# Performance work log

Hardware: AMD Instinct MI355X
Metric: run time of the kernel (lower is better)

## Reference

```python
import jax, jax.numpy as jnp
import numpy as np


def setup_inputs() -> dict:
    key = jax.random.key(0)
    k1, k2, k3 = jax.random.split(key, 3)
    B, K, OUT, IN = 8192, 8, 1024, 1024
    bound = (6.0 / (IN * OUT)) ** 0.5
    x = jax.random.normal(k1, (B, IN), dtype=jnp.float32)
    expert_weights = jax.random.uniform(k2, (B, K), dtype=jnp.float32)
    weight = jax.random.uniform(k3, (K, OUT, IN), dtype=jnp.float32, minval=-bound, maxval=bound)
    bias = jnp.zeros((K, OUT), dtype=jnp.float32)
    return {"x": x, "expert_weights": expert_weights, "weight": weight, "bias": bias}


def reference(x, expert_weights, weight, bias):
    # Mathematically identical to: blended_W = einsum('bk,koi->boi'); bmm(blended_W, x)
    # but avoids materializing the [B,out,in] intermediate: apply each expert's
    # linear map then blend with routing weights (contraction reassociation).
    per_expert = jnp.einsum('bi,koi->bko', x, weight)        # [B, K, out]
    y = jnp.einsum('bk,bko->bo', expert_weights, per_expert)  # [B, out]
    y = y + expert_weights @ bias                             # blended bias [B, out]
    return y
```

## Files before the change

### kernel.cpp

```cpp
#include <hip/hip_runtime.h>
#include <hip/hip_bf16.h>

typedef __attribute__((ext_vector_type(8))) short short8;
typedef __attribute__((ext_vector_type(4))) float f32x4;

#define NDIM 1024
#define INDIM 1024
#define KEXP 8
#define BROWS 8192
#define NX (BROWS * INDIM)
#define NW (KEXP * NDIM * INDIM)

__device__ __forceinline__ unsigned int pack2bf(float a, float b) {
    __hip_bfloat162 h = __float22bfloat162_rn(make_float2(a, b));
    union { __hip_bfloat162 h; unsigned int u; } cv;
    cv.h = h;
    return cv.u;
}

__device__ __forceinline__ void gload16(const void* src, void* ldsdst) {
    __builtin_amdgcn_global_load_lds(
        (__attribute__((address_space(1))) void*)(src),
        (__attribute__((address_space(3))) void*)(ldsdst), 16, 0, 0);
}

__global__ void convert_bf16(const float* __restrict__ x, const float* __restrict__ w,
                             unsigned short* __restrict__ dst) {
    const long total = (long)NX + NW;
    const long stride = (long)gridDim.x * blockDim.x * 8;
    for (long i = ((long)blockIdx.x * blockDim.x + threadIdx.x) * 8; i < total; i += stride) {
        const float* s = (i < NX) ? (x + i) : (w + (i - NX));
        float4 a = ((const float4*)s)[0];
        float4 b = ((const float4*)s)[1];
        uint4 q;
        q.x = pack2bf(a.x, a.y); q.y = pack2bf(a.z, a.w);
        q.z = pack2bf(b.x, b.y); q.w = pack2bf(b.z, b.w);
        *(uint4*)(dst + i) = q;
    }
}

__global__ __launch_bounds__(512, 2)
void moe_gemm_fold(const unsigned short* __restrict__ xb,
                   const float* __restrict__ ew,
                   const unsigned short* __restrict__ Wp,
                   const float* __restrict__ bias,
                   float* __restrict__ out) {
    __shared__ __align__(16) unsigned short lds[2 * 32768];

    const int tid = threadIdx.x;
    const int bid = blockIdx.x;
    const int xcd = bid & 7;
    const int grp = bid >> 3;
    const int bt = xcd * 4 + (grp & 3);
    const int ot = grp >> 2;
    const int bbase = bt * 256;
    const int o_blk = ot * 32;

    const int w  = tid >> 6;
    const int l  = tid & 63;
    const int lr = l & 15;
    const int lg = l >> 4;
    const int wrow = (w >> 2) * 128;
    const int wcol = (w & 3) * 64;

    const int lrow = l >> 2;
    const int sg = (l & 3) ^ ((l >> 3) & 3);
    const int swz = (lr >> 1) & 3;

    int aoff[8][2], boff[4][2];
#pragma unroll
    for (int mf = 0; mf < 8; ++mf)
#pragma unroll
        for (int ks = 0; ks < 2; ++ks)
            aoff[mf][ks] = ks * 8192 + (wrow + mf * 16 + lr) * 32 + ((lg ^ swz) * 8);
#pragma unroll
    for (int nf = 0; nf < 4; ++nf)
#pragma unroll
        for (int ks = 0; ks < 2; ++ks)
            boff[nf][ks] = 16384 + ks * 8192 + (wcol + nf * 16 + lr) * 32 + ((lg ^ swz) * 8);

    auto stage4 = [&](int slot, int kt, int half) {
#pragma unroll
        for (int i = 0; i < 4; ++i) {
            const int id = w * 8 + half * 4 + i;
            unsigned short* dst = &lds[slot * 32768 + id * 512];
            const int sub = id & 15;
            const int col = kt * 64 + ((id >> 4) & 1) * 32 + sg * 8;
            if (id < 32) {
                gload16(Wp + (size_t)(lrow & 7) * (NDIM * INDIM)
                           + (size_t)(o_blk + sub * 2 + (lrow >> 3)) * INDIM + col, dst);
            } else {
                gload16(xb + (size_t)(bbase + sub * 16 + lrow) * INDIM + col, dst);
            }
        }
    };

    f32x4 acc[8][4];
#pragma unroll
    for (int mf = 0; mf < 8; ++mf)
#pragma unroll
        for (int nf = 0; nf < 4; ++nf) acc[mf][nf] = f32x4{0.f, 0.f, 0.f, 0.f};

    stage4(0, 0, 0);
    stage4(0, 0, 1);

#pragma unroll 1
    for (int kt = 0; kt < 16; ++kt) {
        const int cs = kt & 1;
        const bool doS = (kt + 1) < 16;

        asm volatile("s_waitcnt vmcnt(0)\n\ts_barrier" ::: "memory");

        const unsigned short* lb = &lds[cs * 32768];
        short8 alo[4], ahi[4], b0[4], b1[4];

#pragma unroll
        for (int m = 0; m < 4; ++m) alo[m] = *(const short8*)(lb + aoff[m][0]);
#pragma unroll
        for (int n = 0; n < 4; ++n) b0[n] = *(const short8*)(lb + boff[n][0]);
        if (doS) stage4(cs ^ 1, kt + 1, 0);
#pragma unroll
        for (int m = 0; m < 4; ++m) ahi[m] = *(const short8*)(lb + aoff[4 + m][0]);

        __builtin_amdgcn_s_setprio(1);
#pragma unroll
        for (int m = 0; m < 4; ++m)
#pragma unroll
            for (int n = 0; n < 4; ++n)
                acc[m][n] = __builtin_amdgcn_mfma_f32_16x16x32_bf16(alo[m], b0[n], acc[m][n], 0, 0, 0);
        __builtin_amdgcn_s_setprio(0);

#pragma unroll
        for (int n = 0; n < 4; ++n) b1[n] = *(const short8*)(lb + boff[n][1]);
#pragma unroll
        for (int m = 0; m < 4; ++m) alo[m] = *(const short8*)(lb + aoff[m][1]);
        if (doS) stage4(cs ^ 1, kt + 1, 1);

        __builtin_amdgcn_s_setprio(1);
#pragma unroll
        for (int m = 0; m < 4; ++m)
#pragma unroll
            for (int n = 0; n < 4; ++n)
                acc[4 + m][n] = __builtin_amdgcn_mfma_f32_16x16x32_bf16(ahi[m], b0[n], acc[4 + m][n], 0, 0, 0);
        __builtin_amdgcn_s_setprio(0);

#pragma unroll
        for (int m = 0; m < 4; ++m) ahi[m] = *(const short8*)(lb + aoff[4 + m][1]);

        __builtin_amdgcn_s_setprio(1);
#pragma unroll
        for (int m = 0; m < 4; ++m)
#pragma unroll
            for (int n = 0; n < 4; ++n)
                acc[m][n] = __builtin_amdgcn_mfma_f32_16x16x32_bf16(alo[m], b1[n], acc[m][n], 0, 0, 0);
        __builtin_amdgcn_s_setprio(0);

        __builtin_amdgcn_s_setprio(1);
#pragma unroll
        for (int m = 0; m < 4; ++m)
#pragma unroll
            for (int n = 0; n < 4; ++n)
                acc[4 + m][n] = __builtin_amdgcn_mfma_f32_16x16x32_bf16(ahi[m], b1[n], acc[4 + m][n], 0, 0, 0);
        __builtin_amdgcn_s_setprio(0);
    }

    __syncthreads();
    float* ylds = (float*)lds;

    const int obw = wrow >> 3;
#pragma unroll
    for (int nf = 0; nf < 4; ++nf) {
        const int bl = wcol + nf * 16 + lr;
        const int bsw = 4 * (bl & 7);
        const float4 ea = *(const float4*)(ew + (size_t)(bbase + bl) * KEXP);
        const float4 eb = *(const float4*)(ew + (size_t)(bbase + bl) * KEXP + 4);
        float c0, c1, c2, c3;
        if (lg & 1) { c0 = eb.x; c1 = eb.y; c2 = eb.z; c3 = eb.w; }
        else        { c0 = ea.x; c1 = ea.y; c2 = ea.z; c3 = ea.w; }
#pragma unroll
        for (int mf = 0; mf < 8; ++mf) {
            float p = c0 * acc[mf][nf][0] + c1 * acc[mf][nf][1]
                    + c2 * acc[mf][nf][2] + c3 * acc[mf][nf][3];
            p += __shfl_xor(p, 16);
            if (!(lg & 1)) {
                const int ol = obw + mf * 2 + (lg >> 1);
                ylds[bl * 32 + (ol ^ bsw)] = p;
            }
        }
    }
    __syncthreads();

    {
        const int b = tid >> 1;
        const int oh = (tid & 1) * 16;
        const int sw = 4 * (b & 7);
        const float* yr = &ylds[b * 32];
        float y0[16];
#pragma unroll
        for (int q = 0; q < 4; ++q) {
            const float4 v = *(const float4*)(yr + ((oh + q * 4) ^ sw));
            y0[q * 4 + 0] = v.x; y0[q * 4 + 1] = v.y;
            y0[q * 4 + 2] = v.z; y0[q * 4 + 3] = v.w;
        }
        const float4 ea = *(const float4*)(ew + (size_t)(bbase + b) * KEXP);
        const float4 e2 = *(const float4*)(ew + (size_t)(bbase + b) * KEXP + 4);
        const float ekk[8] = {ea.x, ea.y, ea.z, ea.w, e2.x, e2.y, e2.z, e2.w};
#pragma unroll
        for (int k = 0; k < 8; ++k) {
            const float* bp = bias + k * NDIM + o_blk + oh;
#pragma unroll
            for (int jj = 0; jj < 16; ++jj) y0[jj] += ekk[k] * bp[jj];
        }
        float* op = out + (size_t)(bbase + b) * NDIM + o_blk + oh;
#pragma unroll
        for (int jj = 0; jj < 4; ++jj)
            *(float4*)(op + jj * 4) =
                make_float4(y0[jj * 4], y0[jj * 4 + 1], y0[jj * 4 + 2], y0[jj * 4 + 3]);
    }
}

#define FLDW 40
__global__ __launch_bounds__(256, 2)
void moe_blend_gemm_fb(const float* __restrict__ x, const float* __restrict__ ew,
                       const float* __restrict__ w, const float* __restrict__ bias,
                       float* __restrict__ out) {
    __shared__ unsigned short lA[128][FLDW];
    __shared__ unsigned short lB[128][FLDW];
    const int tid = threadIdx.x, bid = blockIdx.x;
    const int nt = bid & 7, mt = bid >> 3;
    const int mbase = mt * 128, nbase = nt * 128;
    const int trow = tid >> 1, tcol = (tid & 1) * 16;
    const float* xp = x + (size_t)(mbase + trow) * INDIM + tcol;
    const float* wp = w + (size_t)(nbase + trow) * INDIM + tcol;
    const float* ep = ew + (size_t)(mbase + trow) * KEXP;
    const int wid = tid >> 6, wrB = (wid >> 1) * 64, wcB = (wid & 1) * 64;
    const int l = tid & 63, lr = l & 15, lg = l >> 4;
    f32x4 acc[4][4];
#pragma unroll
    for (int m = 0; m < 4; ++m)
#pragma unroll
        for (int n = 0; n < 4; ++n) acc[m][n] = f32x4{0.f, 0.f, 0.f, 0.f};
    const unsigned short* rdA = &lA[wrB + lr][lg * 8];
    const unsigned short* rdB = &lB[wcB + lr][lg * 8];
    unsigned int* wA = (unsigned int*)&lA[trow][tcol];
    unsigned int* wB = (unsigned int*)&lB[trow][tcol];
    float4 ra0, ra1, ra2, ra3, rb0, rb1, rb2, rb3;
    float sc;
    {
        const float4* pa = (const float4*)(xp);
        ra0 = pa[0]; ra1 = pa[1]; ra2 = pa[2]; ra3 = pa[3];
        const float4* pb = (const float4*)(wp);
        rb0 = pb[0]; rb1 = pb[1]; rb2 = pb[2]; rb3 = pb[3];
        sc = ep[0];
    }
    for (int tt = 0; tt < 256; ++tt) {
        __syncthreads();
        uint4 qa0, qa1, qb0, qb1;
        qa0.x = pack2bf(ra0.x * sc, ra0.y * sc); qa0.y = pack2bf(ra0.z * sc, ra0.w * sc);
        qa0.z = pack2bf(ra1.x * sc, ra1.y * sc); qa0.w = pack2bf(ra1.z * sc, ra1.w * sc);
        qa1.x = pack2bf(ra2.x * sc, ra2.y * sc); qa1.y = pack2bf(ra2.z * sc, ra2.w * sc);
        qa1.z = pack2bf(ra3.x * sc, ra3.y * sc); qa1.w = pack2bf(ra3.z * sc, ra3.w * sc);
        qb0.x = pack2bf(rb0.x, rb0.y); qb0.y = pack2bf(rb0.z, rb0.w);
        qb0.z = pack2bf(rb1.x, rb1.y); qb0.w = pack2bf(rb1.z, rb1.w);
        qb1.x = pack2bf(rb2.x, rb2.y); qb1.y = pack2bf(rb2.z, rb2.w);
        qb1.z = pack2bf(rb3.x, rb3.y); qb1.w = pack2bf(rb3.z, rb3.w);
        *(uint4*)(wA) = qa0; *(uint4*)(wA + 4) = qa1;
        *(uint4*)(wB) = qb0; *(uint4*)(wB + 4) = qb1;
        __syncthreads();
        if (tt + 1 < 256) {
            const int kc = (tt + 1) >> 5, i0 = ((tt + 1) & 31) * 32;
            const float4* pa = (const float4*)(xp + i0);
            ra0 = pa[0]; ra1 = pa[1]; ra2 = pa[2]; ra3 = pa[3];
            const float4* pb = (const float4*)(wp + (size_t)kc * (size_t)(NDIM * INDIM) + i0);
            rb0 = pb[0]; rb1 = pb[1]; rb2 = pb[2]; rb3 = pb[3];
            sc = ep[kc];
        }
        short8 af[4], bf[4];
#pragma unroll
        for (int m = 0; m < 4; ++m) af[m] = *(const short8*)(rdA + m * 16 * FLDW);
#pragma unroll
        for (int n = 0; n < 4; ++n) bf[n] = *(const short8*)(rdB + n * 16 * FLDW);
#pragma unroll
        for (int m = 0; m < 4; ++m)
#pragma unroll
            for (int n = 0; n < 4; ++n)
                acc[m][n] = __builtin_amdgcn_mfma_f32_16x16x32_bf16(af[m], bf[n], acc[m][n], 0, 0, 0);
    }
#pragma unroll
    for (int m = 0; m < 4; ++m)
#pragma unroll
        for (int j = 0; j < 4; ++j) {
            const int gr = mbase + wrB + m * 16 + lg * 4 + j;
            const float4* e4 = (const float4*)(ew + (size_t)gr * KEXP);
            const float4 e0 = e4[0], e1 = e4[1];
            const float eb[8] = {e0.x, e0.y, e0.z, e0.w, e1.x, e1.y, e1.z, e1.w};
            float* op = out + (size_t)gr * NDIM + nbase + wcB;
#pragma unroll
            for (int n = 0; n < 4; ++n) {
                float t = acc[m][n][j];
#pragma unroll
                for (int kk = 0; kk < 8; ++kk) t += eb[kk] * bias[kk * NDIM + nbase + wcB + n * 16 + lr];
                op[n * 16 + lr] = t;
            }
        }
}

extern "C" void kernel_launch(void* const* d_in, const int* in_sizes, int n_in,
                              void* d_out, int out_size, void* d_ws, size_t ws_size,
                              hipStream_t stream) {
    (void)in_sizes; (void)n_in; (void)out_size;
    const float* x    = (const float*)d_in[0];
    const float* ew   = (const float*)d_in[1];
    const float* w    = (const float*)d_in[2];
    const float* bias = (const float*)d_in[3];
    float* out = (float*)d_out;

    const size_t need = (size_t)(NX + NW) * sizeof(unsigned short);

    if (ws_size >= need) {
        unsigned short* xb = (unsigned short*)d_ws;
        unsigned short* Wp = xb + NX;
        hipLaunchKernelGGL(convert_bf16, dim3(4096), dim3(256), 0, stream, x, w, xb);
        hipLaunchKernelGGL(moe_gemm_fold, dim3(1024), dim3(512), 0, stream, xb, ew, Wp, bias, out);
    } else {
        hipLaunchKernelGGL(moe_blend_gemm_fb, dim3(512), dim3(256), 0, stream, x, ew, w, bias, out);
    }
}
```

Before: 146.4 us.

## Make GEMM blocks loop over four output tiles with continuous cross-tile prefetch

The grid shrinks from 1024 to 256 blocks, one per CU. Each block now walks four consecutive 32-wide output tiles in a single 64-step K loop. The double-buffered global-to-LDS prefetch keeps running across tile boundaries, and each tile's expert-blend epilogue runs inline into a separate LDS buffer. This removes per-block prologue and pipeline-drain costs and the wave tail. In exchange, LDS use per block grows, the epilogue now serialises inside the main loop, and fewer blocks are available for latency hiding.

```diff
diff --git a/kernel.cpp b/kernel.cpp
--- a/kernel.cpp
+++ b/kernel.cpp
@@ -40,21 +40,21 @@
 }
 
 __global__ __launch_bounds__(512, 2)
-void moe_gemm_fold(const unsigned short* __restrict__ xb,
-                   const float* __restrict__ ew,
-                   const unsigned short* __restrict__ Wp,
-                   const float* __restrict__ bias,
-                   float* __restrict__ out) {
+void moe_gemm_pf(const unsigned short* __restrict__ xb,
+                 const float* __restrict__ ew,
+                 const unsigned short* __restrict__ Wp,
+                 const float* __restrict__ bias,
+                 float* __restrict__ out) {
     __shared__ __align__(16) unsigned short lds[2 * 32768];
+    __shared__ __align__(16) float ylds[8192];
 
     const int tid = threadIdx.x;
     const int bid = blockIdx.x;
     const int xcd = bid & 7;
-    const int grp = bid >> 3;
-    const int bt = xcd * 4 + (grp & 3);
-    const int ot = grp >> 2;
+    const int bt = xcd * 4 + ((bid >> 3) & 3);
+    const int ogrp = bid >> 5;
     const int bbase = bt * 256;
-    const int o_blk = ot * 32;
+    const int o_base = ogrp * 128;
 
     const int w  = tid >> 6;
     const int l  = tid & 63;
@@ -79,16 +79,18 @@
         for (int ks = 0; ks < 2; ++ks)
             boff[nf][ks] = 16384 + ks * 8192 + (wcol + nf * 16 + lr) * 32 + ((lg ^ swz) * 8);
 
-    auto stage4 = [&](int slot, int kt, int half) {
+    auto stage4 = [&](int slot, int g, int half) {
+        const int o_blk_s = o_base + (g >> 4) * 32;
+        const int kcol = (g & 15) * 64;
 #pragma unroll
         for (int i = 0; i < 4; ++i) {
             const int id = w * 8 + half * 4 + i;
             unsigned short* dst = &lds[slot * 32768 + id * 512];
             const int sub = id & 15;
-            const int col = kt * 64 + ((id >> 4) & 1) * 32 + sg * 8;
+            const int col = kcol + ((id >> 4) & 1) * 32 + sg * 8;
             if (id < 32) {
                 gload16(Wp + (size_t)(lrow & 7) * (NDIM * INDIM)
-                           + (size_t)(o_blk + sub * 2 + (lrow >> 3)) * INDIM + col, dst);
+                           + (size_t)(o_blk_s + sub * 2 + (lrow >> 3)) * INDIM + col, dst);
             } else {
                 gload16(xb + (size_t)(bbase + sub * 16 + lrow) * INDIM + col, dst);
             }
@@ -105,9 +107,9 @@
     stage4(0, 0, 1);
 
 #pragma unroll 1
-    for (int kt = 0; kt < 16; ++kt) {
-        const int cs = kt & 1;
-        const bool doS = (kt + 1) < 16;
+    for (int g = 0; g < 64; ++g) {
+        const int cs = g & 1;
+        const bool doS = (g + 1) < 64;
 
         asm volatile("s_waitcnt vmcnt(0)\n\ts_barrier" ::: "memory");
 
@@ -118,7 +120,7 @@
         for (int m = 0; m < 4; ++m) alo[m] = *(const short8*)(lb + aoff[m][0]);
 #pragma unroll
         for (int n = 0; n < 4; ++n) b0[n] = *(const short8*)(lb + boff[n][0]);
-        if (doS) stage4(cs ^ 1, kt + 1, 0);
+        if (doS) stage4(cs ^ 1, g + 1, 0);
 #pragma unroll
         for (int m = 0; m < 4; ++m) ahi[m] = *(const short8*)(lb + aoff[4 + m][0]);
 
@@ -134,7 +136,7 @@
         for (int n = 0; n < 4; ++n) b1[n] = *(const short8*)(lb + boff[n][1]);
 #pragma unroll
         for (int m = 0; m < 4; ++m) alo[m] = *(const short8*)(lb + aoff[m][1]);
-        if (doS) stage4(cs ^ 1, kt + 1, 1);
+        if (doS) stage4(cs ^ 1, g + 1, 1);
 
         __builtin_amdgcn_s_setprio(1);
 #pragma unroll
@@ -162,60 +164,61 @@
             for (int n = 0; n < 4; ++n)
                 acc[4 + m][n] = __builtin_amdgcn_mfma_f32_16x16x32_bf16(ahi[m], b1[n], acc[4 + m][n], 0, 0, 0);
         __builtin_amdgcn_s_setprio(0);
-    }
-
-    __syncthreads();
-    float* ylds = (float*)lds;
-
-    const int obw = wrow >> 3;
-#pragma unroll
-    for (int nf = 0; nf < 4; ++nf) {
-        const int bl = wcol + nf * 16 + lr;
-        const int bsw = 4 * (bl & 7);
-        const float4 ea = *(const float4*)(ew + (size_t)(bbase + bl) * KEXP);
-        const float4 eb = *(const float4*)(ew + (size_t)(bbase + bl) * KEXP + 4);
-        float c0, c1, c2, c3;
-        if (lg & 1) { c0 = eb.x; c1 = eb.y; c2 = eb.z; c3 = eb.w; }
-        else        { c0 = ea.x; c1 = ea.y; c2 = ea.z; c3 = ea.w; }
-#pragma unroll
-        for (int mf = 0; mf < 8; ++mf) {
-            float p = c0 * acc[mf][nf][0] + c1 * acc[mf][nf][1]
-                    + c2 * acc[mf][nf][2] + c3 * acc[mf][nf][3];
-            p += __shfl_xor(p, 16);
-            if (!(lg & 1)) {
-                const int ol = obw + mf * 2 + (lg >> 1);
-                ylds[bl * 32 + (ol ^ bsw)] = p;
+
+        if ((g & 15) == 15) {
+            const int o_blk = o_base + (g >> 4) * 32;
+            const int obw = wrow >> 3;
+#pragma unroll
+            for (int nf = 0; nf < 4; ++nf) {
+                const int bl = wcol + nf * 16 + lr;
+                const int bsw = 4 * (bl & 7);
+                const float4 ea = *(const float4*)(ew + (size_t)(bbase + bl) * KEXP);
+                const float4 eb = *(const float4*)(ew + (size_t)(bbase + bl) * KEXP + 4);
+                float c0, c1, c2, c3;
+                if (lg & 1) { c0 = eb.x; c1 = eb.y; c2 = eb.z; c3 = eb.w; }
+                else        { c0 = ea.x; c1 = ea.y; c2 = ea.z; c3 = ea.w; }
+#pragma unroll
+                for (int mf = 0; mf < 8; ++mf) {
+                    float p = c0 * acc[mf][nf][0] + c1 * acc[mf][nf][1]
+                            + c2 * acc[mf][nf][2] + c3 * acc[mf][nf][3];
+                    p += __shfl_xor(p, 16);
+                    if (!(lg & 1)) {
+                        const int ol = obw + mf * 2 + (lg >> 1);
+                        ylds[bl * 32 + (ol ^ bsw)] = p;
+                    }
+                    acc[mf][nf] = f32x4{0.f, 0.f, 0.f, 0.f};
+                }
+            }
+            __syncthreads();
+
+            {
+                const int b = tid >> 1;
+                const int oh = (tid & 1) * 16;
+                const int sw = 4 * (b & 7);
+                const float* yr = &ylds[b * 32];
+                float y0[16];
+#pragma unroll
+                for (int q = 0; q < 4; ++q) {
+                    const float4 v = *(const float4*)(yr + ((oh + q * 4) ^ sw));
+                    y0[q * 4 + 0] = v.x; y0[q * 4 + 1] = v.y;
+                    y0[q * 4 + 2] = v.z; y0[q * 4 + 3] = v.w;
+                }
+                const float4 ea = *(const float4*)(ew + (size_t)(bbase + b) * KEXP);
+                const float4 e2 = *(const float4*)(ew + (size_t)(bbase + b) * KEXP + 4);
+                const float ekk[8] = {ea.x, ea.y, ea.z, ea.w, e2.x, e2.y, e2.z, e2.w};
+#pragma unroll
+                for (int k = 0; k < 8; ++k) {
+                    const float* bp = bias + k * NDIM + o_blk + oh;
+#pragma unroll
+                    for (int jj = 0; jj < 16; ++jj) y0[jj] += ekk[k] * bp[jj];
+                }
+                float* op = out + (size_t)(bbase + b) * NDIM + o_blk + oh;
+#pragma unroll
+                for (int jj = 0; jj < 4; ++jj)
+                    *(float4*)(op + jj * 4) =
+                        make_float4(y0[jj * 4], y0[jj * 4 + 1], y0[jj * 4 + 2], y0[jj * 4 + 3]);
             }
         }
-    }
-    __syncthreads();
-
-    {
-        const int b = tid >> 1;
-        const int oh = (tid & 1) * 16;
-        const int sw = 4 * (b & 7);
-        const float* yr = &ylds[b * 32];
-        float y0[16];
-#pragma unroll
-        for (int q = 0; q < 4; ++q) {
-            const float4 v = *(const float4*)(yr + ((oh + q * 4) ^ sw));
-            y0[q * 4 + 0] = v.x; y0[q * 4 + 1] = v.y;
-            y0[q * 4 + 2] = v.z; y0[q * 4 + 3] = v.w;
-        }
-        const float4 ea = *(const float4*)(ew + (size_t)(bbase + b) * KEXP);
-        const float4 e2 = *(const float4*)(ew + (size_t)(bbase + b) * KEXP + 4);
-        const float ekk[8] = {ea.x, ea.y, ea.z, ea.w, e2.x, e2.y, e2.z, e2.w};
-#pragma unroll
-        for (int k = 0; k < 8; ++k) {
-            const float* bp = bias + k * NDIM + o_blk + oh;
-#pragma unroll
-            for (int jj = 0; jj < 16; ++jj) y0[jj] += ekk[k] * bp[jj];
-        }
-        float* op = out + (size_t)(bbase + b) * NDIM + o_blk + oh;
-#pragma unroll
-        for (int jj = 0; jj < 4; ++jj)
-            *(float4*)(op + jj * 4) =
-                make_float4(y0[jj * 4], y0[jj * 4 + 1], y0[jj * 4 + 2], y0[jj * 4 + 3]);
     }
 }
 
@@ -321,7 +324,7 @@
         unsigned short* xb = (unsigned short*)d_ws;
         unsigned short* Wp = xb + NX;
         hipLaunchKernelGGL(convert_bf16, dim3(4096), dim3(256), 0, stream, x, w, xb);
-        hipLaunchKernelGGL(moe_gemm_fold, dim3(1024), dim3(512), 0, stream, xb, ew, Wp, bias, out);
+        hipLaunchKernelGGL(moe_gemm_pf, dim3(256), dim3(512), 0, stream, xb, ew, Wp, bias, out);
     } else {
         hipLaunchKernelGGL(moe_blend_gemm_fb, dim3(512), dim3(256), 0, stream, x, ew, w, bias, out);
     }
```

Result: slower. 215.2 us (+47.0%).
